# Optimization experiments

Hardware: AMD Instinct MI355X
Metric: run time of the kernel (lower is better)

## Reference

```python
import jax, jax.numpy as jnp
import numpy as np

EPS = 1e-5  # torch InstanceNorm3d default


def setup_inputs() -> dict:
    key = jax.random.key(0)
    k1, k2, k3 = jax.random.split(key, 3)
    B, Cin, Cout, T, D, H, W = 1, 32, 64, 2, 48, 48, 48
    x = jax.random.normal(k1, (B, Cin, T, D, H, W), dtype=jnp.float32)
    # Conv4d 'hypercube' kernel: full 3x3x3x3 over (T, D, H, W)
    Wk = jax.random.normal(k2, (Cout, Cin, 3, 3, 3, 3), dtype=jnp.float32) * 0.02
    b = jax.random.normal(k3, (Cout,), dtype=jnp.float32) * 0.02
    return {"x": x, "Wk": Wk, "b": b}


def _forward(x, Wk, b):
    # Per-time-slice InstanceNorm3d (affine=False): normalize over (D,H,W)
    # independently for each (batch, channel, t). Vectorized over t.
    mean = jnp.mean(x, axis=(-3, -2, -1), keepdims=True)
    var = jnp.var(x, axis=(-3, -2, -1), keepdims=True)  # biased, as torch
    h = (x - mean) * jax.lax.rsqrt(var + EPS)
    # Activation (ReLU)
    h = jax.nn.relu(h)
    # Conv4d over spatial dims (T, D, H, W), padding=1, stride 1 + bias.
    dn = jax.lax.ConvDimensionNumbers(
        lhs_spec=(0, 1, 2, 3, 4, 5),  # N, C, T, D, H, W
        rhs_spec=(0, 1, 2, 3, 4, 5),  # O, I, kT, kD, kH, kW
        out_spec=(0, 1, 2, 3, 4, 5),
    )
    out = jax.lax.conv_general_dilated(
        h, Wk,
        window_strides=(1, 1, 1, 1),
        padding=[(1, 1)] * 4,
        dimension_numbers=dn,
    )
    out = out + b[None, :, None, None, None, None]
    # Dropout with drop_rate=0 -> Identity; the per-slice stack is a no-op.
    return out


def reference(x, Wk, b):
    return _forward(x, Wk, b)
```

## Files before the change

### kernel.cpp

```cpp
#include <hip/hip_runtime.h>

namespace {

typedef unsigned short u16;
typedef __attribute__((ext_vector_type(8))) short short8;
typedef __attribute__((ext_vector_type(4))) float f32x4;
typedef __attribute__((ext_vector_type(4))) unsigned int u32x4;

constexpr int kD = 48;
constexpr int kSliceN = kD * kD * kD;
constexpr int kP = 8;

constexpr int SHR1 = 0x111;
constexpr int SHL1 = 0x101;
constexpr int SHL15 = 0x10F;
constexpr int SHR15 = 0x11F;

__device__ inline u16 f2bf(float f) {
  unsigned u = __float_as_uint(f);
  u += 0x7fffu + ((u >> 16) & 1u);
  return (u16)(u >> 16);
}

__device__ inline void gl_lds16(const void* g, void* l) {
  __builtin_amdgcn_global_load_lds(
      (const __attribute__((address_space(1))) unsigned int*)g,
      (__attribute__((address_space(3))) unsigned int*)l, 16, 0, 0);
}

template <int CM>
__device__ inline short8 dpp4(short8 m) {
  u32x4 mu = __builtin_bit_cast(u32x4, m), r;
  #pragma unroll
  for (int j = 0; j < 4; ++j)
    r[j] = (unsigned)__builtin_amdgcn_update_dpp(0, (int)mu[j], CM, 0xf, 0xf, true);
  return __builtin_bit_cast(short8, r);
}
template <int CM, int CP>
__device__ inline short8 dpp4p(short8 m, short8 nb, bool pl) {
  u32x4 mu = __builtin_bit_cast(u32x4, m), nu = __builtin_bit_cast(u32x4, nb), r;
  #pragma unroll
  for (int j = 0; j < 4; ++j) {
    unsigned a = (unsigned)__builtin_amdgcn_update_dpp(0, (int)mu[j], CM, 0xf, 0xf, true);
    unsigned b = (unsigned)__builtin_amdgcn_update_dpp(0, (int)nu[j], CP, 0xf, 0xf, true);
    r[j] = pl ? b : a;
  }
  return __builtin_bit_cast(short8, r);
}

#define MFMA16(A, B, C) __builtin_amdgcn_mfma_f32_16x16x32_bf16((A), (B), (C), 0, 0, 0)

__global__ __launch_bounds__(256) void k_stats_partial(const float* __restrict__ x,
                                                       float* __restrict__ part) {
  const int slice = blockIdx.x >> 3;
  const int p = blockIdx.x & 7;
  const float4* base = reinterpret_cast<const float4*>(x + (size_t)slice * kSliceN);
  const int per = (kSliceN / 4) / kP;
  const int start = p * per;
  float s = 0.f, sq = 0.f;
  for (int i = start + (int)threadIdx.x; i < start + per; i += 256) {
    float4 v = base[i];
    s += (v.x + v.y) + (v.z + v.w);
    sq += (v.x * v.x + v.y * v.y) + (v.z * v.z + v.w * v.w);
  }
  #pragma unroll
  for (int off = 32; off > 0; off >>= 1) {
    s += __shfl_down(s, off);
    sq += __shfl_down(sq, off);
  }
  __shared__ float red[2][4];
  const int wave = threadIdx.x >> 6;
  if ((threadIdx.x & 63) == 0) { red[0][wave] = s; red[1][wave] = sq; }
  __syncthreads();
  if (threadIdx.x == 0) {
    s = (red[0][0] + red[0][1]) + (red[0][2] + red[0][3]);
    sq = (red[1][0] + red[1][1]) + (red[1][2] + red[1][3]);
    part[blockIdx.x * 2 + 0] = s;
    part[blockIdx.x * 2 + 1] = sq;
  }
}

__global__ __launch_bounds__(256) void k_wtrans(const float* __restrict__ wk,
                                                u16* __restrict__ wt) {
  __shared__ float lw[2592];
  const int co = blockIdx.x;
  const int tid = threadIdx.x;
  const float4* src = reinterpret_cast<const float4*>(wk + (size_t)co * 2592);
  #pragma unroll
  for (int k = 0; k < 3; ++k) {
    const int i = tid + k * 256;
    if (i < 648) ((float4*)lw)[i] = src[i];
  }
  __syncthreads();
  for (int g = tid; g < 324; g += 256) {
    const int tap = g >> 2, kcg = g & 3;
    u32x4 o;
    #pragma unroll
    for (int j = 0; j < 4; ++j) {
      const unsigned lo = f2bf(lw[(kcg * 8 + 2 * j + 0) * 81 + tap]);
      const unsigned hi = f2bf(lw[(kcg * 8 + 2 * j + 1) * 81 + tap]);
      o[j] = lo | (hi << 16);
    }
    *(u32x4*)(wt + (size_t)tap * 2048 + co * 32 + kcg * 8) = o;
  }
}

__global__ __launch_bounds__(256) void k_norm(const float* __restrict__ x,
                                              const float* __restrict__ part,
                                              u16* __restrict__ xn) {
  __shared__ u16 ls[6 * 1536];
  __shared__ float sm[32], sr[32];
  const int tid = threadIdx.x;
  const int bid = blockIdx.x;
  const int hs = bid & 7;
  const int dz = (bid >> 3) % 48;
  const int t = bid / 384;
  const int hy0 = hs * 6;

  if (tid < 32) {
    const int slice = tid * 2 + t;
    float s = 0.f, sq = 0.f;
    #pragma unroll
    for (int p = 0; p < kP; ++p) {
      s += part[(slice * kP + p) * 2 + 0];
      sq += part[(slice * kP + p) * 2 + 1];
    }
    const float inv_n = 1.0f / (float)kSliceN;
    const float mean = s * inv_n;
    const float var = sq * inv_n - mean * mean;
    sm[tid] = mean;
    sr[tid] = rsqrtf(var + 1e-5f);
  }
  __syncthreads();

  #pragma unroll
  for (int k = 0; k < 9; ++k) {
    const int F = tid + k * 256;
    const int ci = F / 72;
    const int rem = F - ci * 72;
    const int hy = rem / 12;
    const int wc = rem - hy * 12;
    const float4 v = *reinterpret_cast<const float4*>(
        x + (size_t)(ci * 2 + t) * 110592 + dz * 2304 + (hy0 + hy) * 48 + wc * 4);
    const float mean = sm[ci], rstd = sr[ci];
    const unsigned a0 = f2bf(fmaxf((v.x - mean) * rstd, 0.f));
    const unsigned a1 = f2bf(fmaxf((v.y - mean) * rstd, 0.f));
    const unsigned a2 = f2bf(fmaxf((v.z - mean) * rstd, 0.f));
    const unsigned a3 = f2bf(fmaxf((v.w - mean) * rstd, 0.f));
    uint2 pk;
    pk.x = a0 | (a1 << 16);
    pk.y = a2 | (a3 << 16);
    *reinterpret_cast<uint2*>(ls + hy * 1536 + ci * 48 + wc * 4) = pk;
  }
  __syncthreads();

  const size_t rb = ((size_t)(t * 48 + dz) * 48 + hy0) * 1536;
  #pragma unroll
  for (int k = 0; k < 5; ++k) {
    const int g = tid + k * 256;
    if (g >= 1152) break;
    const int hy = g / 192;
    const int rem = g - hy * 192;
    const int kcg = rem / 48;
    const int w = rem - kcg * 48;
    const u16* base = ls + hy * 1536 + w;
    u32x4 o;
    #pragma unroll
    for (int j = 0; j < 4; ++j) {
      const unsigned lo = base[(kcg * 8 + 2 * j + 0) * 48];
      const unsigned hi = base[(kcg * 8 + 2 * j + 1) * 48];
      o[j] = lo | (hi << 16);
    }
    const int q = w >> 2;
    const int gd = q * 16 + ((kcg ^ (q & 3)) << 2) + (w & 3);
    *(u32x4*)(xn + rb + (size_t)hy * 1536 + gd * 8) = o;
  }
}

__global__ __launch_bounds__(256, 4) void k_conv(const u16* __restrict__ xn,
                                                 const u16* __restrict__ wt,
                                                 const float* __restrict__ bias,
                                                 float* __restrict__ out) {
  __shared__ u16 xs[12 * 1536];
  const int tid = threadIdx.x, wid = tid >> 6, lane = tid & 63;
  const int r15 = lane & 15, kc = lane >> 4;

  const int orig = blockIdx.x;
  const int swz = (orig & 7) * 144 + (orig >> 3);
  const int to = swz & 1;
  const int ht = (swz >> 1) % 12;
  const int dz = swz / 24;
  const int h0 = ht * 4;

  {
    f32x4 z = {0.f, 0.f, 0.f, 0.f};
    f32x4* p = (f32x4*)xs;
    #pragma unroll
    for (int k = 0; k < 9; ++k) p[tid + k * 256] = z;
  }

  int grano[3];
  #pragma unroll
  for (int wf = 0; wf < 3; ++wf) {
    const int w = wf * 16 + r15, q = w >> 2;
    grano[wf] = (q * 16 + ((kc ^ (q & 3)) << 2) + (w & 3)) << 4;
  }
  const bool pl0 = (r15 == 0), pl15 = (r15 == 15);

  f32x4 acc[4][3];
  #pragma unroll
  for (int m = 0; m < 4; ++m)
    #pragma unroll
    for (int wf = 0; wf < 3; ++wf) acc[m][wf] = (f32x4){0.f, 0.f, 0.f, 0.f};

  __syncthreads();

  for (int dd = 0; dd < 3; ++dd) {
    const int din = dz + dd - 1;
    const bool vd = (din >= 0) && (din < 48);
    if (vd) {
      for (int u = wid; u < 12; u += 4) {
        const int tin = u / 6, hh = u - tin * 6;
        const int hin = h0 - 1 + hh;
        if (hin < 0 || hin >= 48) continue;
        const u16* src = xn + ((size_t)((tin * 48 + din) * 48 + hin)) * 1536 + lane * 8;
        u16* dstb = xs + u * 1536;
        #pragma unroll
        for (int p = 0; p < 3; ++p) gl_lds16(src + p * 512, dstb + p * 512);
      }
    }
    __syncthreads();
    if (vd) {
      #pragma unroll
      for (int tin = 0; tin < 2; ++tin) {
        const int kt = tin + 1 - to;
        #pragma unroll
        for (int half = 0; half < 2; ++half) {
          short8 xr[4][3];
          #pragma unroll
          for (int ri = 0; ri < 4; ++ri) {
            const char* rb = (const char*)(xs + (tin * 6 + 2 * half + ri) * 1536);
            #pragma unroll
            for (int wf = 0; wf < 3; ++wf)
              xr[ri][wf] = *(const short8*)(rb + grano[wf]);
          }
          #pragma unroll
          for (int kh = 0; kh < 3; ++kh) {
            const int tapb = ((kt * 3 + dd) * 3 + kh) * 3;
            short8 wB[3];
            #pragma unroll
            for (int kw = 0; kw < 3; ++kw)
              wB[kw] = *(const short8*)(wt + (size_t)(tapb + kw) * 2048 + wid * 512 +
                                        r15 * 32 + kc * 8);
            #pragma unroll
            for (int mr = 0; mr < 2; ++mr) {
              const int m = 2 * half + mr;
              const short8 aC0 = xr[mr + kh][0], aC1 = xr[mr + kh][1], aC2 = xr[mr + kh][2];
              const short8 aL0 = dpp4<SHR1>(aC0);
              const short8 aL1 = dpp4p<SHR1, SHL15>(aC1, aC0, pl0);
              const short8 aL2 = dpp4p<SHR1, SHL15>(aC2, aC1, pl0);
              const short8 aR0 = dpp4p<SHL1, SHR15>(aC0, aC1, pl15);
              const short8 aR1 = dpp4p<SHL1, SHR15>(aC1, aC2, pl15);
              const short8 aR2 = dpp4<SHL1>(aC2);
              acc[m][0] = MFMA16(wB[0], aL0, acc[m][0]);
              acc[m][0] = MFMA16(wB[1], aC0, acc[m][0]);
              acc[m][0] = MFMA16(wB[2], aR0, acc[m][0]);
              acc[m][1] = MFMA16(wB[0], aL1, acc[m][1]);
              acc[m][1] = MFMA16(wB[1], aC1, acc[m][1]);
              acc[m][1] = MFMA16(wB[2], aR1, acc[m][1]);
              acc[m][2] = MFMA16(wB[0], aL2, acc[m][2]);
              acc[m][2] = MFMA16(wB[1], aC2, acc[m][2]);
              acc[m][2] = MFMA16(wB[2], aR2, acc[m][2]);
            }
          }
        }
      }
    }
    __syncthreads();
  }

  float bv[4];
  #pragma unroll
  for (int j = 0; j < 4; ++j) bv[j] = bias[wid * 16 + kc * 4 + j];
  #pragma unroll
  for (int m = 0; m < 4; ++m) {
    const int hy = h0 + m;
    float* ob = out + (size_t)to * 110592 + (size_t)dz * 2304 + (size_t)hy * 48;
    #pragma unroll
    for (int wf = 0; wf < 3; ++wf) {
      const int w = wf * 16 + r15;
      #pragma unroll
      for (int j = 0; j < 4; ++j) {
        const int co = wid * 16 + kc * 4 + j;
        ob[(size_t)co * 221184 + w] = acc[m][wf][j] + bv[j];
      }
    }
  }
}

}

extern "C" void kernel_launch(void* const* d_in, const int* in_sizes, int n_in,
                              void* d_out, int out_size, void* d_ws, size_t ws_size,
                              hipStream_t stream) {
  const float* x = (const float*)d_in[0];
  const float* wk = (const float*)d_in[1];
  const float* bias = (const float*)d_in[2];
  float* out = (float*)d_out;

  float* part = (float*)d_ws;
  u16* xn = (u16*)((char*)d_ws + 4096);
  u16* wt = xn + 7077888;

  k_stats_partial<<<dim3(512), dim3(256), 0, stream>>>(x, part);
  k_wtrans<<<dim3(64), dim3(256), 0, stream>>>(wk, wt);
  k_norm<<<dim3(768), dim3(256), 0, stream>>>(x, part, xn);
  k_conv<<<dim3(1152), dim3(256), 0, stream>>>(xn, wt, bias, out);
}
```

Measured before the change: 150.5 us.

## Enlarge conv H-tile to six rows and merge stats with weight transform

The conv kernel now computes six output rows per block instead of four, staging eight halo rows per time slice. It loads the nine weight fragments per kh once per time slice and reuses each loaded activation row across all kh taps, which cuts halo overhead and redundant LDS and weight loads. Grid size drops from 1152 to 768 blocks and occupancy is lowered to 3 blocks per CU, since more accumulators and LDS are needed per block. The stats and weight-transform kernels are fused into a single launch to save one kernel dispatch.

```diff
diff --git a/kernel.cpp b/kernel.cpp
--- a/kernel.cpp
+++ b/kernel.cpp
@@ -50,15 +50,42 @@
 
 #define MFMA16(A, B, C) __builtin_amdgcn_mfma_f32_16x16x32_bf16((A), (B), (C), 0, 0, 0)
 
-__global__ __launch_bounds__(256) void k_stats_partial(const float* __restrict__ x,
-                                                       float* __restrict__ part) {
-  const int slice = blockIdx.x >> 3;
-  const int p = blockIdx.x & 7;
+__global__ __launch_bounds__(256) void k_prep(const float* __restrict__ x,
+                                              const float* __restrict__ wk,
+                                              float* __restrict__ part,
+                                              u16* __restrict__ wt) {
+  const int tid = threadIdx.x;
+  if (blockIdx.x < 64) {
+    __shared__ float lw[2592];
+    const int co = blockIdx.x;
+    const float4* src = reinterpret_cast<const float4*>(wk + (size_t)co * 2592);
+    #pragma unroll
+    for (int k = 0; k < 3; ++k) {
+      const int i = tid + k * 256;
+      if (i < 648) ((float4*)lw)[i] = src[i];
+    }
+    __syncthreads();
+    for (int g = tid; g < 324; g += 256) {
+      const int tap = g >> 2, kcg = g & 3;
+      u32x4 o;
+      #pragma unroll
+      for (int j = 0; j < 4; ++j) {
+        const unsigned lo = f2bf(lw[(kcg * 8 + 2 * j + 0) * 81 + tap]);
+        const unsigned hi = f2bf(lw[(kcg * 8 + 2 * j + 1) * 81 + tap]);
+        o[j] = lo | (hi << 16);
+      }
+      *(u32x4*)(wt + (size_t)tap * 2048 + co * 32 + kcg * 8) = o;
+    }
+    return;
+  }
+  const int sbid = blockIdx.x - 64;
+  const int slice = sbid >> 3;
+  const int p = sbid & 7;
   const float4* base = reinterpret_cast<const float4*>(x + (size_t)slice * kSliceN);
   const int per = (kSliceN / 4) / kP;
   const int start = p * per;
   float s = 0.f, sq = 0.f;
-  for (int i = start + (int)threadIdx.x; i < start + per; i += 256) {
+  for (int i = start + tid; i < start + per; i += 256) {
     float4 v = base[i];
     s += (v.x + v.y) + (v.z + v.w);
     sq += (v.x * v.x + v.y * v.y) + (v.z * v.z + v.w * v.w);
@@ -69,39 +96,14 @@
     sq += __shfl_down(sq, off);
   }
   __shared__ float red[2][4];
-  const int wave = threadIdx.x >> 6;
-  if ((threadIdx.x & 63) == 0) { red[0][wave] = s; red[1][wave] = sq; }
+  const int wave = tid >> 6;
+  if ((tid & 63) == 0) { red[0][wave] = s; red[1][wave] = sq; }
   __syncthreads();
-  if (threadIdx.x == 0) {
+  if (tid == 0) {
     s = (red[0][0] + red[0][1]) + (red[0][2] + red[0][3]);
     sq = (red[1][0] + red[1][1]) + (red[1][2] + red[1][3]);
-    part[blockIdx.x * 2 + 0] = s;
-    part[blockIdx.x * 2 + 1] = sq;
-  }
-}
-
-__global__ __launch_bounds__(256) void k_wtrans(const float* __restrict__ wk,
-                                                u16* __restrict__ wt) {
-  __shared__ float lw[2592];
-  const int co = blockIdx.x;
-  const int tid = threadIdx.x;
-  const float4* src = reinterpret_cast<const float4*>(wk + (size_t)co * 2592);
-  #pragma unroll
-  for (int k = 0; k < 3; ++k) {
-    const int i = tid + k * 256;
-    if (i < 648) ((float4*)lw)[i] = src[i];
-  }
-  __syncthreads();
-  for (int g = tid; g < 324; g += 256) {
-    const int tap = g >> 2, kcg = g & 3;
-    u32x4 o;
-    #pragma unroll
-    for (int j = 0; j < 4; ++j) {
-      const unsigned lo = f2bf(lw[(kcg * 8 + 2 * j + 0) * 81 + tap]);
-      const unsigned hi = f2bf(lw[(kcg * 8 + 2 * j + 1) * 81 + tap]);
-      o[j] = lo | (hi << 16);
-    }
-    *(u32x4*)(wt + (size_t)tap * 2048 + co * 32 + kcg * 8) = o;
+    part[sbid * 2 + 0] = s;
+    part[sbid * 2 + 1] = sq;
   }
 }
 
@@ -177,26 +179,26 @@
   }
 }
 
-__global__ __launch_bounds__(256, 4) void k_conv(const u16* __restrict__ xn,
+__global__ __launch_bounds__(256, 3) void k_conv(const u16* __restrict__ xn,
                                                  const u16* __restrict__ wt,
                                                  const float* __restrict__ bias,
                                                  float* __restrict__ out) {
-  __shared__ u16 xs[12 * 1536];
+  __shared__ u16 xs[16 * 1536];
   const int tid = threadIdx.x, wid = tid >> 6, lane = tid & 63;
   const int r15 = lane & 15, kc = lane >> 4;
 
   const int orig = blockIdx.x;
-  const int swz = (orig & 7) * 144 + (orig >> 3);
+  const int swz = (orig & 7) * 96 + (orig >> 3);
   const int to = swz & 1;
-  const int ht = (swz >> 1) % 12;
-  const int dz = swz / 24;
-  const int h0 = ht * 4;
+  const int ht = (swz >> 1) & 7;
+  const int dz = swz >> 4;
+  const int h0 = ht * 6;
 
   {
     f32x4 z = {0.f, 0.f, 0.f, 0.f};
     f32x4* p = (f32x4*)xs;
     #pragma unroll
-    for (int k = 0; k < 9; ++k) p[tid + k * 256] = z;
+    for (int k = 0; k < 12; ++k) p[tid + k * 256] = z;
   }
 
   int grano[3];
@@ -207,9 +209,9 @@
   }
   const bool pl0 = (r15 == 0), pl15 = (r15 == 15);
 
-  f32x4 acc[4][3];
-  #pragma unroll
-  for (int m = 0; m < 4; ++m)
+  f32x4 acc[6][3];
+  #pragma unroll
+  for (int m = 0; m < 6; ++m)
     #pragma unroll
     for (int wf = 0; wf < 3; ++wf) acc[m][wf] = (f32x4){0.f, 0.f, 0.f, 0.f};
 
@@ -219,9 +221,9 @@
     const int din = dz + dd - 1;
     const bool vd = (din >= 0) && (din < 48);
     if (vd) {
-      for (int u = wid; u < 12; u += 4) {
-        const int tin = u / 6, hh = u - tin * 6;
-        const int hin = h0 - 1 + hh;
+      for (int u = wid; u < 16; u += 4) {
+        const int tin = u >> 3, rr = u & 7;
+        const int hin = h0 - 1 + rr;
         if (hin < 0 || hin >= 48) continue;
         const u16* src = xn + ((size_t)((tin * 48 + din) * 48 + hin)) * 1536 + lane * 8;
         u16* dstb = xs + u * 1536;
@@ -234,44 +236,39 @@
       #pragma unroll
       for (int tin = 0; tin < 2; ++tin) {
         const int kt = tin + 1 - to;
+        short8 wB[3][3];
         #pragma unroll
-        for (int half = 0; half < 2; ++half) {
-          short8 xr[4][3];
+        for (int kh = 0; kh < 3; ++kh)
           #pragma unroll
-          for (int ri = 0; ri < 4; ++ri) {
-            const char* rb = (const char*)(xs + (tin * 6 + 2 * half + ri) * 1536);
-            #pragma unroll
-            for (int wf = 0; wf < 3; ++wf)
-              xr[ri][wf] = *(const short8*)(rb + grano[wf]);
-          }
+          for (int kw = 0; kw < 3; ++kw)
+            wB[kh][kw] = *(const short8*)(wt +
+                (size_t)(((kt * 3 + dd) * 3 + kh) * 3 + kw) * 2048 +
+                wid * 512 + r15 * 32 + kc * 8);
+        #pragma unroll
+        for (int r = 0; r < 8; ++r) {
+          const char* rb = (const char*)(xs + (tin * 8 + r) * 1536);
+          const short8 aC0 = *(const short8*)(rb + grano[0]);
+          const short8 aC1 = *(const short8*)(rb + grano[1]);
+          const short8 aC2 = *(const short8*)(rb + grano[2]);
+          const short8 aL0 = dpp4<SHR1>(aC0);
+          const short8 aL1 = dpp4p<SHR1, SHL15>(aC1, aC0, pl0);
+          const short8 aL2 = dpp4p<SHR1, SHL15>(aC2, aC1, pl0);
+          const short8 aR0 = dpp4p<SHL1, SHR15>(aC0, aC1, pl15);
+          const short8 aR1 = dpp4p<SHL1, SHR15>(aC1, aC2, pl15);
+          const short8 aR2 = dpp4<SHL1>(aC2);
           #pragma unroll
           for (int kh = 0; kh < 3; ++kh) {
-            const int tapb = ((kt * 3 + dd) * 3 + kh) * 3;
-            short8 wB[3];
-            #pragma unroll
-            for (int kw = 0; kw < 3; ++kw)
-              wB[kw] = *(const short8*)(wt + (size_t)(tapb + kw) * 2048 + wid * 512 +
-                                        r15 * 32 + kc * 8);
-            #pragma unroll
-            for (int mr = 0; mr < 2; ++mr) {
-              const int m = 2 * half + mr;
-              const short8 aC0 = xr[mr + kh][0], aC1 = xr[mr + kh][1], aC2 = xr[mr + kh][2];
-              const short8 aL0 = dpp4<SHR1>(aC0);
-              const short8 aL1 = dpp4p<SHR1, SHL15>(aC1, aC0, pl0);
-              const short8 aL2 = dpp4p<SHR1, SHL15>(aC2, aC1, pl0);
-              const short8 aR0 = dpp4p<SHL1, SHR15>(aC0, aC1, pl15);
-              const short8 aR1 = dpp4p<SHL1, SHR15>(aC1, aC2, pl15);
-              const short8 aR2 = dpp4<SHL1>(aC2);
-              acc[m][0] = MFMA16(wB[0], aL0, acc[m][0]);
-              acc[m][0] = MFMA16(wB[1], aC0, acc[m][0]);
-              acc[m][0] = MFMA16(wB[2], aR0, acc[m][0]);
-              acc[m][1] = MFMA16(wB[0], aL1, acc[m][1]);
-              acc[m][1] = MFMA16(wB[1], aC1, acc[m][1]);
-              acc[m][1] = MFMA16(wB[2], aR1, acc[m][1]);
-              acc[m][2] = MFMA16(wB[0], aL2, acc[m][2]);
-              acc[m][2] = MFMA16(wB[1], aC2, acc[m][2]);
-              acc[m][2] = MFMA16(wB[2], aR2, acc[m][2]);
-            }
+            const int m = r - kh;
+            if (m < 0 || m > 5) continue;
+            acc[m][0] = MFMA16(wB[kh][0], aL0, acc[m][0]);
+            acc[m][0] = MFMA16(wB[kh][1], aC0, acc[m][0]);
+            acc[m][0] = MFMA16(wB[kh][2], aR0, acc[m][0]);
+            acc[m][1] = MFMA16(wB[kh][0], aL1, acc[m][1]);
+            acc[m][1] = MFMA16(wB[kh][1], aC1, acc[m][1]);
+            acc[m][1] = MFMA16(wB[kh][2], aR1, acc[m][1]);
+            acc[m][2] = MFMA16(wB[kh][0], aL2, acc[m][2]);
+            acc[m][2] = MFMA16(wB[kh][1], aC2, acc[m][2]);
+            acc[m][2] = MFMA16(wB[kh][2], aR2, acc[m][2]);
           }
         }
       }
@@ -283,7 +280,7 @@
   #pragma unroll
   for (int j = 0; j < 4; ++j) bv[j] = bias[wid * 16 + kc * 4 + j];
   #pragma unroll
-  for (int m = 0; m < 4; ++m) {
+  for (int m = 0; m < 6; ++m) {
     const int hy = h0 + m;
     float* ob = out + (size_t)to * 110592 + (size_t)dz * 2304 + (size_t)hy * 48;
     #pragma unroll
@@ -312,8 +309,7 @@
   u16* xn = (u16*)((char*)d_ws + 4096);
   u16* wt = xn + 7077888;
 
-  k_stats_partial<<<dim3(512), dim3(256), 0, stream>>>(x, part);
-  k_wtrans<<<dim3(64), dim3(256), 0, stream>>>(wk, wt);
+  k_prep<<<dim3(576), dim3(256), 0, stream>>>(x, wk, part, wt);
   k_norm<<<dim3(768), dim3(256), 0, stream>>>(x, part, xn);
-  k_conv<<<dim3(1152), dim3(256), 0, stream>>>(xn, wt, bias, out);
-}
+  k_conv<<<dim3(768), dim3(256), 0, stream>>>(xn, wt, bias, out);
+}
```

Measured after the change: 139.5 us. 1.08x faster.
